# Kernel optimization log

Measured on AMD Instinct MI355X. Metric: run time of the kernel, lower is better.

The kernel has to match this reference:

```python
import jax, jax.numpy as jnp
import numpy as np

SCALING = 2.0  # alpha / r = 128 / 64


def setup_inputs() -> dict:
    key = jax.random.key(0)
    k1, k2, k3, k4 = jax.random.split(key, 4)
    in_f, out_f, r, tokens = 4096, 16384, 64, 64
    return {
        "x": jax.random.normal(k1, (tokens, in_f), dtype=jnp.float32),
        "weight": jax.random.normal(k2, (out_f, in_f), dtype=jnp.float32) * (1.0 / np.sqrt(in_f)),
        "lora_A": jax.random.normal(k3, (r, in_f), dtype=jnp.float32) * (1.0 / np.sqrt(in_f)),
        "lora_B": jax.random.normal(k4, (out_f, r), dtype=jnp.float32) * (1.0 / np.sqrt(r)),
    }


def reference(x, weight, lora_A, lora_B):
    # base GEMM: [T, in] @ [in, out] -> [T, out]
    base = x @ weight.T
    # low-rank adapter: ((x @ A^T) @ B^T) scaled
    lora = (x @ lora_A.T) @ lora_B.T
    return base + SCALING * lora
```

## Files before the change

kernel.cpp:

```cpp
#include <hip/hip_runtime.h>
#include <hip/hip_bf16.h>

typedef __attribute__((ext_vector_type(8))) short bf16x8;
typedef __attribute__((ext_vector_type(4))) float f32x4;

__device__ __forceinline__ short f2b(float f) {
    __hip_bfloat16 h = __float2bfloat16(f);
    return __builtin_bit_cast(short, h);
}

#define NPH 32
#define KC  128

__global__ void prep_kernel(const float* __restrict__ x,
                            const float* __restrict__ A,
                            ushort* __restrict__ xb,
                            ushort* __restrict__ yb) {
    const int tid = threadIdx.x, bid = blockIdx.x;

    const int gid = bid * 256 + tid;
    if (gid < 65536) {
        float4 v = ((const float4*)x)[gid];
        ushort4 s;
        s.x = (ushort)f2b(v.x); s.y = (ushort)f2b(v.y);
        s.z = (ushort)f2b(v.z); s.w = (ushort)f2b(v.w);
        ((ushort4*)xb)[gid] = s;
    }

    const int wave = tid >> 6, lane = tid & 63;
    const int idx = bid * 4 + wave;
    const int t = idx >> 6, r = idx & 63;
    const float4* xr = (const float4*)(x + (size_t)t * 4096);
    const float4* ar = (const float4*)(A + (size_t)r * 4096);
    float s = 0.f;
    #pragma unroll
    for (int i = 0; i < 16; ++i) {
        float4 a = xr[i * 64 + lane];
        float4 b = ar[i * 64 + lane];
        s += a.x * b.x + a.y * b.y + a.z * b.z + a.w * b.w;
    }
    #pragma unroll
    for (int off = 32; off; off >>= 1) s += __shfl_xor(s, off, 64);
    if (lane == 0) yb[idx] = (ushort)f2b(2.0f * s);
}

__global__ void __launch_bounds__(512)
lora_gemm(const float* __restrict__ W,
          const float* __restrict__ Bm,
          const ushort* __restrict__ xb,
          const ushort* __restrict__ yb,
          float* __restrict__ out) {
    __shared__ char buf[4][64 * 512];

    const int tid  = threadIdx.x;
    const int w    = tid >> 6;
    const int lane = tid & 63;
    const int j0   = blockIdx.x << 6;

    if (w >= 4) {
        const int s = w - 4;
        auto issue = [&](int p) {
            char* dst = &buf[p & 3][0];
            #pragma unroll
            for (int i = 0; i < 8; ++i) {
                const int qa = s * 16 + i * 2;
                const int q  = qa + (lane >> 5);
                const int b  = (lane & 31) * 16;
                const char* src = (const char*)(W + (size_t)(j0 + q) * 4096
                                                + (size_t)p * KC)
                                  + (b ^ ((q & 7) << 4));
                __builtin_amdgcn_global_load_lds(
                    (const uint32_t*)src,
                    (uint32_t*)(dst + qa * 512), 16, 0, 0);
            }
        };

        issue(0);
        issue(1);
        issue(2);
        for (int p = 0; p < NPH - 2; ++p) {
            asm volatile("s_waitcnt vmcnt(16)" ::: "memory");
            __builtin_amdgcn_s_barrier();
            if (p + 3 < NPH) issue(p + 3);
        }
        asm volatile("s_waitcnt vmcnt(8)" ::: "memory");
        __builtin_amdgcn_s_barrier();
        asm volatile("s_waitcnt vmcnt(0)" ::: "memory");
        __builtin_amdgcn_s_barrier();
        return;
    }

    const int c  = lane & 15;
    const int kg = lane >> 4;
    const ushort* xrow = xb + (size_t)(w * 16 + c) * 4096 + kg * 8;

    f32x4 acc[4];
    #pragma unroll
    for (int n = 0; n < 4; ++n) acc[n] = f32x4{0.f, 0.f, 0.f, 0.f};

    for (int p = 0; p < NPH; ++p) {
        __builtin_amdgcn_s_barrier();
        const char* lb = &buf[p & 3][0];
        #pragma unroll
        for (int sl = 0; sl < 4; ++sl) {
            bf16x8 aa = *(const bf16x8*)(xrow + p * KC + sl * 32);
            #pragma unroll
            for (int n = 0; n < 4; ++n) {
                const int q   = n * 16 + c;
                const int swz = (q & 7) << 4;
                const char* base = lb + q * 512;
                f32x4 w0 = *(const f32x4*)(base + ((sl * 128 + kg * 32) ^ swz));
                f32x4 w1 = *(const f32x4*)(base + ((sl * 128 + kg * 32 + 16) ^ swz));
                bf16x8 bb;
                bb[0] = f2b(w0[0]); bb[1] = f2b(w0[1]);
                bb[2] = f2b(w0[2]); bb[3] = f2b(w0[3]);
                bb[4] = f2b(w1[0]); bb[5] = f2b(w1[1]);
                bb[6] = f2b(w1[2]); bb[7] = f2b(w1[3]);
                acc[n] = __builtin_amdgcn_mfma_f32_16x16x32_bf16(
                    aa, bb, acc[n], 0, 0, 0);
            }
        }
    }

    {
        const ushort* y0 = yb + (size_t)(w * 16 + c) * 64 + kg * 8;
        #pragma unroll
        for (int n = 0; n < 4; ++n) {
            const float* br = Bm + (size_t)(j0 + n * 16 + c) * 64 + kg * 8;
            #pragma unroll
            for (int k = 0; k < 64; k += 32) {
                f32x4 w0 = *(const f32x4*)(br + k);
                f32x4 w1 = *(const f32x4*)(br + k + 4);
                bf16x8 bb;
                bb[0] = f2b(w0[0]); bb[1] = f2b(w0[1]);
                bb[2] = f2b(w0[2]); bb[3] = f2b(w0[3]);
                bb[4] = f2b(w1[0]); bb[5] = f2b(w1[1]);
                bb[6] = f2b(w1[2]); bb[7] = f2b(w1[3]);
                bf16x8 aa = *(const bf16x8*)(y0 + k);
                acc[n] = __builtin_amdgcn_mfma_f32_16x16x32_bf16(
                    aa, bb, acc[n], 0, 0, 0);
            }
        }
    }

    #pragma unroll
    for (int n = 0; n < 4; ++n) {
        float* op = out + j0 + n * 16 + c;
        #pragma unroll
        for (int r = 0; r < 4; ++r)
            op[(size_t)(w * 16 + kg * 4 + r) * 16384] = acc[n][r];
    }
}

extern "C" void kernel_launch(void* const* d_in, const int* in_sizes, int n_in,
                              void* d_out, int out_size, void* d_ws, size_t ws_size,
                              hipStream_t stream) {
    const float* x  = (const float*)d_in[0];
    const float* W  = (const float*)d_in[1];
    const float* A  = (const float*)d_in[2];
    const float* Bm = (const float*)d_in[3];
    float* out = (float*)d_out;

    ushort* xb = (ushort*)d_ws;
    ushort* yb = (ushort*)((char*)d_ws + 524288);

    prep_kernel<<<1024, 256, 0, stream>>>(x, A, xb, yb);
    lora_gemm<<<256, 512, 0, stream>>>(W, Bm, xb, yb, out);
}
```

Measured before the change: 63.92 us.

## Use larger K chunks with double buffering and staggered per-block K start

The W streaming pipeline moves from four 128-wide K stages to two 256-wide stages, each producer load now covering a full 1KB row segment. Each block starts its K loop at a different offset (blockIdx & 15) to spread DRAM/L2 accesses across blocks. A second barrier per stage replaces the earlier buffer reuse guard. Only two stages are in flight, so prefetch depth drops while per-stage bytes double, and the extra barrier adds sync cost.

```diff
diff --git a/kernel.cpp b/kernel.cpp
--- a/kernel.cpp
+++ b/kernel.cpp
@@ -9,8 +9,8 @@
     return __builtin_bit_cast(short, h);
 }
 
-#define NPH 32
-#define KC  128
+#define NSP 16
+#define KCS 256
 
 __global__ void prep_kernel(const float* __restrict__ x,
                             const float* __restrict__ A,
@@ -50,43 +50,43 @@
           const ushort* __restrict__ xb,
           const ushort* __restrict__ yb,
           float* __restrict__ out) {
-    __shared__ char buf[4][64 * 512];
+    __shared__ char buf[2][64 * 1024];
 
     const int tid  = threadIdx.x;
     const int w    = tid >> 6;
     const int lane = tid & 63;
     const int j0   = blockIdx.x << 6;
+    const int p0   = blockIdx.x & 15;
 
     if (w >= 4) {
-        const int s = w - 4;
-        auto issue = [&](int p) {
-            char* dst = &buf[p & 3][0];
+        const int s16 = (w - 4) * 16;
+        auto issue = [&](int i) {
+            const int sp = (p0 + i) & 15;
+            char* dst = &buf[i & 1][0];
             #pragma unroll
-            for (int i = 0; i < 8; ++i) {
-                const int qa = s * 16 + i * 2;
-                const int q  = qa + (lane >> 5);
-                const int b  = (lane & 31) * 16;
+            for (int k = 0; k < 16; ++k) {
+                const int q = s16 + k;
                 const char* src = (const char*)(W + (size_t)(j0 + q) * 4096
-                                                + (size_t)p * KC)
-                                  + (b ^ ((q & 7) << 4));
+                                                + (size_t)sp * KCS)
+                                  + ((lane * 16) ^ ((k & 7) << 4));
                 __builtin_amdgcn_global_load_lds(
                     (const uint32_t*)src,
-                    (uint32_t*)(dst + qa * 512), 16, 0, 0);
+                    (uint32_t*)(dst + q * 1024), 16, 0, 0);
             }
         };
 
         issue(0);
         issue(1);
-        issue(2);
-        for (int p = 0; p < NPH - 2; ++p) {
-            asm volatile("s_waitcnt vmcnt(16)" ::: "memory");
+        for (int i = 0; i < NSP; ++i) {
+            if (i + 1 < NSP) {
+                asm volatile("s_waitcnt vmcnt(16)" ::: "memory");
+            } else {
+                asm volatile("s_waitcnt vmcnt(0)" ::: "memory");
+            }
             __builtin_amdgcn_s_barrier();
-            if (p + 3 < NPH) issue(p + 3);
+            __builtin_amdgcn_s_barrier();
+            if (i + 2 < NSP) issue(i + 2);
         }
-        asm volatile("s_waitcnt vmcnt(8)" ::: "memory");
-        __builtin_amdgcn_s_barrier();
-        asm volatile("s_waitcnt vmcnt(0)" ::: "memory");
-        __builtin_amdgcn_s_barrier();
         return;
     }
 
@@ -98,28 +98,36 @@
     #pragma unroll
     for (int n = 0; n < 4; ++n) acc[n] = f32x4{0.f, 0.f, 0.f, 0.f};
 
-    for (int p = 0; p < NPH; ++p) {
+    for (int i = 0; i < NSP; ++i) {
+        const int sp = (p0 + i) & 15;
         __builtin_amdgcn_s_barrier();
-        const char* lb = &buf[p & 3][0];
+        const char* lb = &buf[i & 1][0];
         #pragma unroll
-        for (int sl = 0; sl < 4; ++sl) {
-            bf16x8 aa = *(const bf16x8*)(xrow + p * KC + sl * 32);
+        for (int half = 0; half < 2; ++half) {
             #pragma unroll
-            for (int n = 0; n < 4; ++n) {
-                const int q   = n * 16 + c;
-                const int swz = (q & 7) << 4;
-                const char* base = lb + q * 512;
-                f32x4 w0 = *(const f32x4*)(base + ((sl * 128 + kg * 32) ^ swz));
-                f32x4 w1 = *(const f32x4*)(base + ((sl * 128 + kg * 32 + 16) ^ swz));
-                bf16x8 bb;
-                bb[0] = f2b(w0[0]); bb[1] = f2b(w0[1]);
-                bb[2] = f2b(w0[2]); bb[3] = f2b(w0[3]);
-                bb[4] = f2b(w1[0]); bb[5] = f2b(w1[1]);
-                bb[6] = f2b(w1[2]); bb[7] = f2b(w1[3]);
-                acc[n] = __builtin_amdgcn_mfma_f32_16x16x32_bf16(
-                    aa, bb, acc[n], 0, 0, 0);
+            for (int sl = 0; sl < 4; ++sl) {
+                bf16x8 aa = *(const bf16x8*)(xrow + sp * KCS
+                                             + half * 128 + sl * 32);
+                #pragma unroll
+                for (int n = 0; n < 4; ++n) {
+                    const int q   = n * 16 + c;
+                    const int swz = (q & 7) << 4;
+                    const char* base = lb + q * 1024 + half * 512;
+                    f32x4 w0 = *(const f32x4*)(base
+                                    + ((sl * 128 + kg * 32) ^ swz));
+                    f32x4 w1 = *(const f32x4*)(base
+                                    + ((sl * 128 + kg * 32 + 16) ^ swz));
+                    bf16x8 bb;
+                    bb[0] = f2b(w0[0]); bb[1] = f2b(w0[1]);
+                    bb[2] = f2b(w0[2]); bb[3] = f2b(w0[3]);
+                    bb[4] = f2b(w1[0]); bb[5] = f2b(w1[1]);
+                    bb[6] = f2b(w1[2]); bb[7] = f2b(w1[3]);
+                    acc[n] = __builtin_amdgcn_mfma_f32_16x16x32_bf16(
+                        aa, bb, acc[n], 0, 0, 0);
+                }
             }
         }
+        __builtin_amdgcn_s_barrier();
     }
 
     {
```

Measured after the change: 82.14 us. +28.5%, slower.
